# Optimization experiments

Hardware: AMD Instinct MI355X
Metric: run time of the kernel (lower is better)

Reference implementation:

```python
import math
import jax, jax.numpy as jnp
import numpy as np

B, S, HID = 2, 2048, 1024
NH, HD = 16, 64            # num heads, head dim (HID = NH*HD)
NB, MAXD = 32, 128         # relative attention buckets / max distance
Q_SCALING = 1.0


def setup_inputs() -> dict:
    key = jax.random.key(0)
    ks = jax.random.split(key, 6)
    return {
        "hidden_states": jax.random.normal(ks[0], (B, S, HID), dtype=jnp.float32),
        "w_qkv": jax.random.normal(ks[1], (HID, 3 * HID), dtype=jnp.float32) * 0.02,
        "b_qkv": jax.random.normal(ks[2], (3 * HID,), dtype=jnp.float32) * 0.02,
        "w_dense": jax.random.normal(ks[3], (HID, HID), dtype=jnp.float32) * 0.02,
        "b_dense": jax.random.normal(ks[4], (HID,), dtype=jnp.float32) * 0.02,
        "rel_attn_table": jax.random.normal(ks[5], (NH, NB), dtype=jnp.float32) * 0.02,
    }


def _relative_position_bucket(q_len, k_len, num_buckets, max_distance):
    # Bidirectional T5-style buckets, matching compute_relative_bias.
    ctx = jnp.arange(q_len, dtype=jnp.int32)[:, None]
    mem = jnp.arange(k_len, dtype=jnp.int32)[None, :]
    rel = mem - ctx                                     # [Q, K]
    nb = num_buckets // 2
    buckets = jnp.where(rel > 0, nb, 0)
    rel = jnp.abs(rel)
    max_exact = nb // 2
    is_small = rel < max_exact
    # log path (clamp to >=1 to avoid log(0); masked by is_small anyway)
    tmp = jnp.log(jnp.maximum(rel, 1).astype(jnp.float32) / max_exact)
    large = tmp / math.log(max_distance / max_exact) * (nb - max_exact)
    large = max_exact + large.astype(jnp.int32)
    large = jnp.minimum(large, nb - 1)
    return buckets + jnp.where(is_small, rel, large)    # [Q, K]


def reference(hidden_states, w_qkv, b_qkv, w_dense, b_dense, rel_attn_table):
    b, s, _ = hidden_states.shape
    qkv = hidden_states @ w_qkv + b_qkv                 # [B, S, 3*HID]
    q, k, v = jnp.split(qkv, 3, axis=-1)
    q = q.reshape(b, s, NH, HD)
    k = k.reshape(b, s, NH, HD)
    v = v.reshape(b, s, NH, HD)

    norm = Q_SCALING * math.sqrt(HD)
    scores = jnp.einsum("bqhd,bkhd->bhqk", q, k) / norm  # [B, H, S, S]

    buckets = _relative_position_bucket(s, s, NB, MAXD)  # [Q, K] int32
    bias = rel_attn_table[:, buckets]                    # [H, Q, K]
    scores = scores + bias[None]

    probs = jax.nn.softmax(scores, axis=-1)
    ctx = jnp.einsum("bhqk,bkhd->bqhd", probs, v).reshape(b, s, HID)
    return ctx @ w_dense + b_dense
```

## Files before the change

### kernel.cpp

```cpp
#include <hip/hip_runtime.h>
#include <hip/hip_bf16.h>
#include <math.h>

#define S_ 2048

typedef __attribute__((ext_vector_type(8))) short bf16x8;
typedef __attribute__((ext_vector_type(4))) float f32x4;
typedef __attribute__((ext_vector_type(8))) unsigned short u16x8;
typedef __attribute__((ext_vector_type(4))) unsigned short u16x4;

__device__ inline unsigned short f2bf(float f) {
  union { float f; unsigned u; } x; x.f = f;
  unsigned r = x.u + 0x7fff + ((x.u >> 16) & 1);
  return (unsigned short)(r >> 16);
}

__device__ __forceinline__ float exp2_raw(float x) {
  float r;
  asm("v_exp_f32 %0, %1" : "=v"(r) : "v"(x));
  return r;
}

__device__ __forceinline__ void gll16(const unsigned short* g, unsigned short* l) {
  __builtin_amdgcn_global_load_lds(
      (const __attribute__((address_space(1))) unsigned int*)g,
      (__attribute__((address_space(3))) unsigned int*)l, 16, 0, 0);
}

__device__ __forceinline__ void transpose_tile(
    const float* __restrict__ in, unsigned short* __restrict__ out,
    int K, int N, int bx, int by, int tid, unsigned short (*tile)[72]) {
  const int k0 = by * 64, n0 = bx * 64;
  const int rr = tid >> 4, cc = (tid & 15) * 4;
#pragma unroll
  for (int p = 0; p < 4; ++p) {
    int k = rr + p * 16;
    float4 v = *(const float4*)&in[(size_t)(k0 + k) * N + n0 + cc];
    tile[k][cc + 0] = f2bf(v.x);
    tile[k][cc + 1] = f2bf(v.y);
    tile[k][cc + 2] = f2bf(v.z);
    tile[k][cc + 3] = f2bf(v.w);
  }
  __syncthreads();
#pragma unroll
  for (int p = 0; p < 4; ++p) {
    int n = rr + p * 16;
    u16x4 o;
    o[0] = tile[cc + 0][n];
    o[1] = tile[cc + 1][n];
    o[2] = tile[cc + 2][n];
    o[3] = tile[cc + 3][n];
    *(u16x4*)&out[(size_t)(n0 + n) * K + k0 + cc] = o;
  }
}

__global__ __launch_bounds__(256) void prologue_kernel(
    const float* __restrict__ hs, unsigned short* __restrict__ hsb,
    const float* __restrict__ w_qkv, unsigned short* __restrict__ wqT,
    const float* __restrict__ w_dense, unsigned short* __restrict__ wdT,
    const float* __restrict__ table, float* __restrict__ biasTab) {
  __shared__ unsigned short tile[64][72];
  const int blk = blockIdx.x;
  const int tid = threadIdx.x;
  if (blk < 2048) {
    int i = blk * 256 + tid;
    float4 a = ((const float4*)hs)[i * 2];
    float4 b = ((const float4*)hs)[i * 2 + 1];
    u16x8 o;
    o[0] = f2bf(a.x); o[1] = f2bf(a.y); o[2] = f2bf(a.z); o[3] = f2bf(a.w);
    o[4] = f2bf(b.x); o[5] = f2bf(b.y); o[6] = f2bf(b.z); o[7] = f2bf(b.w);
    *(u16x8*)&hsb[(size_t)i * 8] = o;
  } else if (blk < 2816) {
    int t = blk - 2048;
    transpose_tile(w_qkv, wqT, 1024, 3072, t % 48, t / 48, tid, tile);
  } else if (blk < 3072) {
    int t = blk - 2816;
    transpose_tile(w_dense, wdT, 1024, 1024, t % 16, t / 16, tid, tile);
  } else {
    int idx = (blk - 3072) * 256 + tid;
    int h = idx >> 12;
    int r = idx & 4095;
    int rel = r - 2047;
    int bucket = rel > 0 ? 16 : 0;
    int ar = rel < 0 ? -rel : rel;
    if (ar < 8) {
      bucket += ar;
    } else {
      float tmp = logf((float)ar / 8.0f);
      float lf = tmp / 2.7725887222397811f * 8.0f;
      int large = 8 + (int)lf;
      bucket += (large < 15 ? large : 15);
    }
    biasTab[idx] = table[h * 32 + bucket] * 1.44269504088896f;
  }
}

template <bool BF16OUT>
__global__ __launch_bounds__(256) void gemm_mfma_kernel(
    const unsigned short* __restrict__ A, const unsigned short* __restrict__ Bt,
    const float* __restrict__ bias, void* __restrict__ Cout,
    unsigned short* __restrict__ vP, int M, int N, int K) {
  __shared__ __align__(16) unsigned short As[2 * 128 * 32];
  __shared__ __align__(16) unsigned short Bs[2 * 128 * 32];
  const int tid = threadIdx.x;
  const int wave = tid >> 6, lane = tid & 63;
  const int lg = lane >> 4, lr = lane & 15;
  const int nbx = gridDim.x;
  const int flat = blockIdx.y * nbx + blockIdx.x;
  const int cpx = (nbx * gridDim.y) >> 3;
  const int swzid = (flat & 7) * cpx + (flat >> 3);
  const int m0 = (swzid / nbx) * 128, n0 = (swzid % nbx) * 128;
  const int wm = (wave & 1) * 64, wn = (wave >> 1) * 64;

  f32x4 acc[4][4] = {};

  const int r0 = tid >> 2;
  const int sw = ((tid & 3) ^ (r0 & 3)) << 3;
  const unsigned short* aP0 = A + (size_t)(m0 + r0) * K + sw;
  const unsigned short* aP1 = A + (size_t)(m0 + 64 + r0) * K + sw;
  const unsigned short* bP0 = Bt + (size_t)(n0 + r0) * K + sw;
  const unsigned short* bP1 = Bt + (size_t)(n0 + 64 + r0) * K + sw;
  unsigned short* ldsA0 = &As[(tid & ~63) * 8];
  unsigned short* ldsA1 = &As[(256 + (tid & ~63)) * 8];
  unsigned short* ldsB0 = &Bs[(tid & ~63) * 8];
  unsigned short* ldsB1 = &Bs[(256 + (tid & ~63)) * 8];

  const int swz = (lg ^ (lr & 3)) << 3;
  const int NT = K >> 5;

  gll16(aP0, ldsA0);
  gll16(aP1, ldsA1);
  gll16(bP0, ldsB0);
  gll16(bP1, ldsB1);

  for (int ti = 0; ti < NT; ++ti) {
    const int cur = ti & 1;
    __syncthreads();
    if (ti + 1 < NT) {
      const int kt = (ti + 1) << 5;
      const int nb = (cur ^ 1) * 4096;
      gll16(aP0 + kt, ldsA0 + nb);
      gll16(aP1 + kt, ldsA1 + nb);
      gll16(bP0 + kt, ldsB0 + nb);
      gll16(bP1 + kt, ldsB1 + nb);
    }
    const unsigned short* Ab = &As[cur * 4096];
    const unsigned short* Bb = &Bs[cur * 4096];
    bf16x8 af[4], bfr[4];
#pragma unroll
    for (int t = 0; t < 4; ++t) {
      af[t]  = *(const bf16x8*)&Ab[(wm + t * 16 + lr) * 32 + swz];
      bfr[t] = *(const bf16x8*)&Bb[(wn + t * 16 + lr) * 32 + swz];
    }
#pragma unroll
    for (int i = 0; i < 4; ++i)
#pragma unroll
      for (int j = 0; j < 4; ++j)
        acc[i][j] = __builtin_amdgcn_mfma_f32_16x16x32_bf16(
            af[i], bfr[j], acc[i][j], 0, 0, 0);
  }

  float bv[4];
#pragma unroll
  for (int j = 0; j < 4; ++j) bv[j] = bias[n0 + wn + j * 16 + lr];

  if constexpr (BF16OUT) {
    __syncthreads();
    if (n0 < 2048) {
      unsigned short* rp = &As[wave * 1024];
#pragma unroll
      for (int i = 0; i < 4; ++i) {
#pragma unroll
        for (int j = 0; j < 4; ++j) {
          const int cw = ((j + lg) & 3) * 16 + lr;
#pragma unroll
          for (int r = 0; r < 4; ++r)
            rp[(lg * 4 + r) * 64 + cw] = f2bf(acc[i][j][r] + bv[j]);
        }
#pragma unroll
        for (int pass = 0; pass < 2; ++pass) {
          const int row = pass * 8 + (lane >> 3);
          const int cread = ((((lane & 7) >> 1) + (row >> 2)) & 3) * 16 +
                            (lane & 1) * 8;
          u16x8 v = *(const u16x8*)&rp[row * 64 + cread];
          *(u16x8*)&((unsigned short*)Cout)[
              (size_t)(m0 + wm + i * 16 + row) * N + n0 + wn + (lane & 7) * 8] = v;
        }
      }
    } else {
      unsigned short* R = (wave < 2) ? &As[(wave & 1) * 4096]
                                     : &Bs[(wave & 1) * 4096];
#pragma unroll
      for (int i = 0; i < 4; ++i) {
        const int lsv = (i >> 1) * 4 + lg;
        const int ebase = (i & 1) * 4;
#pragma unroll
        for (int j = 0; j < 4; ++j) {
          const int d = j * 16 + lr;
          const int ps = lsv ^ (d & 7);
          u16x4 o;
#pragma unroll
          for (int r = 0; r < 4; ++r) o[r] = f2bf(acc[i][j][r] + bv[j]);
          *(u16x4*)&R[d * 64 + ps * 8 + ebase] = o;
        }
      }
      const int krow0 = m0 + wm;
      const int bbv = krow0 >> 11;
      const int sbase = krow0 & 2047;
      const int h = ((n0 - 2048) >> 6) + (wave >> 1);
#pragma unroll
      for (int it = 0; it < 8; ++it) {
        const int d = it * 8 + (lane >> 3);
        const int c = lane & 7;
        u16x8 v = *(const u16x8*)&R[d * 64 + c * 8];
        *(u16x8*)&vP[((size_t)((bbv * 16 + h) * 64 + d)) * 2048 +
                     sbase + c * 8] = v;
      }
    }
  } else {
#pragma unroll
    for (int i = 0; i < 4; ++i)
#pragma unroll
      for (int j = 0; j < 4; ++j)
#pragma unroll
        for (int r = 0; r < 4; ++r) {
          int row = m0 + wm + i * 16 + lg * 4 + r;
          int col = n0 + wn + j * 16 + lr;
          ((float*)Cout)[(size_t)row * N + col] = acc[i][j][r] + bv[j];
        }
  }
}

template <bool BF16OUT>
__global__ __launch_bounds__(256) void gemm_mfma64_kernel(
    const unsigned short* __restrict__ A, const unsigned short* __restrict__ Bt,
    const float* __restrict__ bias, void* __restrict__ Cout,
    int M, int N, int K) {
  __shared__ __align__(16) unsigned short As[2 * 64 * 32];
  __shared__ __align__(16) unsigned short Bs[2 * 128 * 32];
  const int tid = threadIdx.x;
  const int wave = tid >> 6, lane = tid & 63;
  const int lg = lane >> 4, lr = lane & 15;
  const int nbx = gridDim.x;
  const int flat = blockIdx.y * nbx + blockIdx.x;
  const int cpx = (nbx * gridDim.y) >> 3;
  const int swzid = (flat & 7) * cpx + (flat >> 3);
  const int m0 = (swzid / nbx) * 64, n0 = (swzid % nbx) * 128;
  const int wm = (wave & 1) * 32, wn = (wave >> 1) * 64;

  f32x4 acc[2][4] = {};

  const int r0 = tid >> 2;
  const int sw = ((tid & 3) ^ (r0 & 3)) << 3;
  const unsigned short* aP  = A + (size_t)(m0 + r0) * K + sw;
  const unsigned short* bP0 = Bt + (size_t)(n0 + r0) * K + sw;
  const unsigned short* bP1 = Bt + (size_t)(n0 + 64 + r0) * K + sw;
  unsigned short* ldsA  = &As[(tid & ~63) * 8];
  unsigned short* ldsB0 = &Bs[(tid & ~63) * 8];
  unsigned short* ldsB1 = &Bs[(256 + (tid & ~63)) * 8];

  const int swz = (lg ^ (lr & 3)) << 3;
  const int NT = K >> 5;

  gll16(aP, ldsA);
  gll16(bP0, ldsB0);
  gll16(bP1, ldsB1);

  for (int ti = 0; ti < NT; ++ti) {
    const int cur = ti & 1;
    __syncthreads();
    if (ti + 1 < NT) {
      const int kt = (ti + 1) << 5;
      gll16(aP + kt, ldsA + (cur ^ 1) * 2048);
      gll16(bP0 + kt, ldsB0 + (cur ^ 1) * 4096);
      gll16(bP1 + kt, ldsB1 + (cur ^ 1) * 4096);
    }
    const unsigned short* Ab = &As[cur * 2048];
    const unsigned short* Bb = &Bs[cur * 4096];
    bf16x8 af[2], bfr[4];
#pragma unroll
    for (int t = 0; t < 2; ++t)
      af[t] = *(const bf16x8*)&Ab[(wm + t * 16 + lr) * 32 + swz];
#pragma unroll
    for (int t = 0; t < 4; ++t)
      bfr[t] = *(const bf16x8*)&Bb[(wn + t * 16 + lr) * 32 + swz];
#pragma unroll
    for (int i = 0; i < 2; ++i)
#pragma unroll
      for (int j = 0; j < 4; ++j)
        acc[i][j] = __builtin_amdgcn_mfma_f32_16x16x32_bf16(
            af[i], bfr[j], acc[i][j], 0, 0, 0);
  }

  float bv[4];
#pragma unroll
  for (int j = 0; j < 4; ++j) bv[j] = bias[n0 + wn + j * 16 + lr];
#pragma unroll
  for (int i = 0; i < 2; ++i) {
#pragma unroll
    for (int j = 0; j < 4; ++j) {
#pragma unroll
      for (int r = 0; r < 4; ++r) {
        int row = m0 + wm + i * 16 + lg * 4 + r;
        int col = n0 + wn + j * 16 + lr;
        float val = acc[i][j][r] + bv[j];
        if constexpr (BF16OUT)
          ((unsigned short*)Cout)[(size_t)row * N + col] = f2bf(val);
        else
          ((float*)Cout)[(size_t)row * N + col] = val;
      }
    }
  }
}

__global__ __launch_bounds__(512) void attn_mfma6_kernel(
    const unsigned short* __restrict__ qkvb, const unsigned short* __restrict__ vP,
    const float* __restrict__ biasTab, unsigned short* __restrict__ ctxb) {
  const int wg0 = blockIdx.x;
  const int wg = (wg0 & 7) * 64 + (wg0 >> 3);
  const int qt = wg & 15;
  const int h  = (wg >> 4) & 15;
  const int bb = wg >> 8;

  const int tid = threadIdx.x;
  const int wave = tid >> 6;
  const int lane = tid & 63;
  const int lg = lane >> 4;
  const int lr = lane & 15;

  __shared__ __align__(16) unsigned short Klds[2][4096];
  __shared__ __align__(16) unsigned short Vlds[2][4096];
  __shared__ float biasW[2][192];

  const int q0 = qt * 128;
  const int qw = q0 + wave * 16;
  const float SCL = 0.125f * 1.44269504088896f;
  const float THR = 11.5415603f;

  bf16x8 qf[2];
#pragma unroll
  for (int kh = 0; kh < 2; ++kh)
    qf[kh] = *(const bf16x8*)(qkvb +
        (size_t)(bb * S_ + qw + lr) * 3072 + h * 64 + kh * 32 + lg * 8);

  float mrun = -1e30f;
  float lpart = 0.f;
  f32x4 ov[4] = {};

  const int kk = tid >> 3, kpb = tid & 7;
  const unsigned short* kptr = qkvb + (size_t)(bb * S_ + kk) * 3072 + 1024 +
                               h * 64 + (kpb ^ (kk & 7)) * 8;
  const unsigned short* vptr = vP + ((size_t)((bb * 16 + h) * 64 + (tid >> 3))) * S_ +
                               (tid & 7) * 8;
  const float* btabH = biasTab + h * 4096 + 2047;

  auto nonuni = [&](int tt) {
    int rl = tt * 64 - q0;
    return !((rl - 127 >= 91) || (rl + 63 <= -91));
  };

  gll16(kptr, &Klds[0][(tid & ~63) * 8]);
  gll16(vptr, &Vlds[0][(tid & ~63) * 8]);
  if (nonuni(0) && tid < 192) biasW[0][tid] = btabH[-q0 - 127 + tid];

  for (int t = 0; t < 32; ++t) {
    const int cur = t & 1;
    __syncthreads();

    if (t < 31) {
      const size_t kadv = (size_t)(t + 1) * 64 * 3072;
      gll16(kptr + kadv, &Klds[cur ^ 1][(tid & ~63) * 8]);
      gll16(vptr + (t + 1) * 64, &Vlds[cur ^ 1][(tid & ~63) * 8]);
      if (nonuni(t + 1) && tid < 192)
        biasW[cur ^ 1][tid] = btabH[(t + 1) * 64 - q0 - 127 + tid];
    }

    f32x4 sc[4] = {};
    __builtin_amdgcn_s_setprio(1);
#pragma unroll
    for (int kt = 0; kt < 4; ++kt) {
      const unsigned short* kr = &Klds[cur][(kt * 16 + lr) * 64];
      bf16x8 kf0 = *(const bf16x8*)(kr + ((lg)     ^ (lr & 7)) * 8);
      bf16x8 kf1 = *(const bf16x8*)(kr + ((4 + lg) ^ (lr & 7)) * 8);
      sc[kt] = __builtin_amdgcn_mfma_f32_16x16x32_bf16(kf0, qf[0], sc[kt], 0, 0, 0);
      sc[kt] = __builtin_amdgcn_mfma_f32_16x16x32_bf16(kf1, qf[1], sc[kt], 0, 0, 0);
    }
    __builtin_amdgcn_s_setprio(0);

    bf16x8 vfr[2][4];
#pragma unroll
    for (int kh = 0; kh < 2; ++kh)
#pragma unroll
      for (int db = 0; db < 4; ++db)
        vfr[kh][db] = *(const bf16x8*)&Vlds[cur][
            (db * 16 + lr) * 64 + ((4 * kh + lg) ^ (lr & 7)) * 8];

    float pp[4][4];
    if (nonuni(t)) {
      const int bidx = 127 + lg * 4 - wave * 16 - lr;
#pragma unroll
      for (int kt = 0; kt < 4; ++kt)
#pragma unroll
        for (int r = 0; r < 4; ++r)
          pp[kt][r] = sc[kt][r] * SCL + biasW[cur][bidx + kt * 16 + r];
    } else {
      const float cb = btabH[t * 64 - q0];
#pragma unroll
      for (int kt = 0; kt < 4; ++kt)
#pragma unroll
        for (int r = 0; r < 4; ++r)
          pp[kt][r] = sc[kt][r] * SCL + cb;
    }

    float mx[8];
#pragma unroll
    for (int i = 0; i < 8; ++i)
      mx[i] = fmaxf(pp[i >> 1][(i & 1) * 2], pp[i >> 1][(i & 1) * 2 + 1]);
    float m01 = fmaxf(mx[0], mx[1]), m23 = fmaxf(mx[2], mx[3]);
    float m45 = fmaxf(mx[4], mx[5]), m67 = fmaxf(mx[6], mx[7]);
    float tm = fmaxf(fmaxf(m01, m23), fmaxf(m45, m67));

    if (!__all(tm <= mrun + THR)) {
      tm = fmaxf(tm, __shfl_xor(tm, 16));
      tm = fmaxf(tm, __shfl_xor(tm, 32));
      float mn = fmaxf(mrun, tm);
      float sfv = exp2_raw(mrun - mn);
      mrun = mn;
      lpart *= sfv;
#pragma unroll
      for (int r = 0; r < 4; ++r) {
        float sq = __shfl(sfv, (lane & 48) | (lg * 4 + r));
#pragma unroll
        for (int db = 0; db < 4; ++db) ov[db][r] *= sq;
      }
    }

#pragma unroll
    for (int kt = 0; kt < 4; ++kt)
#pragma unroll
      for (int r = 0; r < 4; ++r)
        pp[kt][r] = exp2_raw(pp[kt][r] - mrun);
    float s8[8];
#pragma unroll
    for (int i = 0; i < 8; ++i)
      s8[i] = pp[i >> 1][(i & 1) * 2] + pp[i >> 1][(i & 1) * 2 + 1];
    float s01 = s8[0] + s8[1], s23 = s8[2] + s8[3];
    float s45 = s8[4] + s8[5], s67 = s8[6] + s8[7];
    lpart += (s01 + s23) + (s45 + s67);

    union { bf16x8 v; unsigned u[4]; } pk[2];
#pragma unroll
    for (int kh = 0; kh < 2; ++kh) {
      asm("v_cvt_pk_bf16_f32 %0, %1, %2"
          : "=v"(pk[kh].u[0]) : "v"(pp[2 * kh][0]), "v"(pp[2 * kh][1]));
      asm("v_cvt_pk_bf16_f32 %0, %1, %2"
          : "=v"(pk[kh].u[1]) : "v"(pp[2 * kh][2]), "v"(pp[2 * kh][3]));
      asm("v_cvt_pk_bf16_f32 %0, %1, %2"
          : "=v"(pk[kh].u[2]) : "v"(pp[2 * kh + 1][0]), "v"(pp[2 * kh + 1][1]));
      asm("v_cvt_pk_bf16_f32 %0, %1, %2"
          : "=v"(pk[kh].u[3]) : "v"(pp[2 * kh + 1][2]), "v"(pp[2 * kh + 1][3]));
    }

    __builtin_amdgcn_s_setprio(1);
#pragma unroll
    for (int kh = 0; kh < 2; ++kh)
#pragma unroll
      for (int db = 0; db < 4; ++db)
        ov[db] = __builtin_amdgcn_mfma_f32_16x16x32_bf16(
            pk[kh].v, vfr[kh][db], ov[db], 0, 0, 0);
    __builtin_amdgcn_s_setprio(0);
  }

  float lsum = lpart;
  lsum += __shfl_xor(lsum, 16);
  lsum += __shfl_xor(lsum, 32);
  float invl = 1.0f / lsum;
#pragma unroll
  for (int r = 0; r < 4; ++r) {
    float iv = __shfl(invl, (lane & 48) | (lg * 4 + r));
    size_t row = (size_t)(bb * S_ + qw + lg * 4 + r);
#pragma unroll
    for (int db = 0; db < 4; ++db)
      ctxb[row * 1024 + h * 64 + db * 16 + lr] = f2bf(ov[db][r] * iv);
  }
}

extern "C" void kernel_launch(void* const* d_in, const int* in_sizes, int n_in,
                              void* d_out, int out_size, void* d_ws, size_t ws_size,
                              hipStream_t stream) {
  const float* hs      = (const float*)d_in[0];
  const float* w_qkv   = (const float*)d_in[1];
  const float* b_qkv   = (const float*)d_in[2];
  const float* w_dense = (const float*)d_in[3];
  const float* b_dense = (const float*)d_in[4];
  const float* rtab    = (const float*)d_in[5];
  float* out = (float*)d_out;

  char* ws = (char*)d_ws;
  unsigned short* qkvb = (unsigned short*)ws;
  unsigned short* ctxb = (unsigned short*)(ws + (((size_t)24) << 20));
  unsigned short* hsb  = (unsigned short*)(ws + (((size_t)32) << 20));
  unsigned short* wqT  = (unsigned short*)(ws + (((size_t)40) << 20));
  unsigned short* wdT  = (unsigned short*)(ws + (((size_t)46) << 20));
  unsigned short* vP   = (unsigned short*)(ws + (((size_t)48) << 20));
  float* biasTab       = (float*)(ws + (((size_t)56) << 20));

  hipLaunchKernelGGL(prologue_kernel, dim3(3328), dim3(256), 0, stream,
                     hs, hsb, w_qkv, wqT, w_dense, wdT, rtab, biasTab);
  hipLaunchKernelGGL((gemm_mfma_kernel<true>), dim3(24, 32), dim3(256), 0, stream,
                     hsb, wqT, b_qkv, (void*)qkvb, vP, 4096, 3072, 1024);
  hipLaunchKernelGGL(attn_mfma6_kernel, dim3(512), dim3(512), 0, stream,
                     qkvb, vP, biasTab, ctxb);
  hipLaunchKernelGGL((gemm_mfma64_kernel<false>), dim3(8, 64), dim3(256), 0, stream,
                     ctxb, wdT, b_dense, (void*)out, 4096, 1024, 1024);
}
```

Baseline: 133.2 us.

## Triple-buffer GEMM LDS tiles with two-deep prefetch and vmcnt waits

Both MFMA GEMM kernels move from double-buffered to triple-buffered LDS staging. Each iteration issues global-to-LDS loads two K-tiles ahead, waits with a partial s_waitcnt vmcnt plus a raw barrier instead of a full __syncthreads, and the bias load is hoisted before the loop. The aim is to hide global load latency behind more MFMA work. In exchange LDS use per block grows by half, which may lower occupancy, and correctness now depends on the hand-written vmcnt counts.

```diff
diff --git a/kernel.cpp b/kernel.cpp
--- a/kernel.cpp
+++ b/kernel.cpp
@@ -100,8 +100,8 @@
     const unsigned short* __restrict__ A, const unsigned short* __restrict__ Bt,
     const float* __restrict__ bias, void* __restrict__ Cout,
     unsigned short* __restrict__ vP, int M, int N, int K) {
-  __shared__ __align__(16) unsigned short As[2 * 128 * 32];
-  __shared__ __align__(16) unsigned short Bs[2 * 128 * 32];
+  __shared__ __align__(16) unsigned short As[3 * 128 * 32];
+  __shared__ __align__(16) unsigned short Bs[3 * 128 * 32];
   const int tid = threadIdx.x;
   const int wave = tid >> 6, lane = tid & 63;
   const int lg = lane >> 4, lr = lane & 15;
@@ -114,38 +114,33 @@
 
   f32x4 acc[4][4] = {};
 
+  float bv[4];
+#pragma unroll
+  for (int j = 0; j < 4; ++j) bv[j] = bias[n0 + wn + j * 16 + lr];
+  asm volatile("" : "+v"(bv[0]), "+v"(bv[1]), "+v"(bv[2]), "+v"(bv[3]));
+
   const int r0 = tid >> 2;
   const int sw = ((tid & 3) ^ (r0 & 3)) << 3;
   const unsigned short* aP0 = A + (size_t)(m0 + r0) * K + sw;
   const unsigned short* aP1 = A + (size_t)(m0 + 64 + r0) * K + sw;
   const unsigned short* bP0 = Bt + (size_t)(n0 + r0) * K + sw;
   const unsigned short* bP1 = Bt + (size_t)(n0 + 64 + r0) * K + sw;
-  unsigned short* ldsA0 = &As[(tid & ~63) * 8];
-  unsigned short* ldsA1 = &As[(256 + (tid & ~63)) * 8];
-  unsigned short* ldsB0 = &Bs[(tid & ~63) * 8];
-  unsigned short* ldsB1 = &Bs[(256 + (tid & ~63)) * 8];
+  const int dstoff = (tid & ~63) * 8;
 
   const int swz = (lg ^ (lr & 3)) << 3;
   const int NT = K >> 5;
 
-  gll16(aP0, ldsA0);
-  gll16(aP1, ldsA1);
-  gll16(bP0, ldsB0);
-  gll16(bP1, ldsB1);
-
-  for (int ti = 0; ti < NT; ++ti) {
-    const int cur = ti & 1;
-    __syncthreads();
-    if (ti + 1 < NT) {
-      const int kt = (ti + 1) << 5;
-      const int nb = (cur ^ 1) * 4096;
-      gll16(aP0 + kt, ldsA0 + nb);
-      gll16(aP1 + kt, ldsA1 + nb);
-      gll16(bP0 + kt, ldsB0 + nb);
-      gll16(bP1 + kt, ldsB1 + nb);
-    }
-    const unsigned short* Ab = &As[cur * 4096];
-    const unsigned short* Bb = &Bs[cur * 4096];
+  auto STAGE = [&](int b, int kt) {
+    unsigned short* Ab = &As[b * 4096];
+    unsigned short* Bb = &Bs[b * 4096];
+    gll16(aP0 + kt, Ab + dstoff);
+    gll16(aP1 + kt, Ab + 2048 + dstoff);
+    gll16(bP0 + kt, Bb + dstoff);
+    gll16(bP1 + kt, Bb + 2048 + dstoff);
+  };
+  auto COMPUTE = [&](int b) {
+    const unsigned short* Ab = &As[b * 4096];
+    const unsigned short* Bb = &Bs[b * 4096];
     bf16x8 af[4], bfr[4];
 #pragma unroll
     for (int t = 0; t < 4; ++t) {
@@ -158,11 +153,25 @@
       for (int j = 0; j < 4; ++j)
         acc[i][j] = __builtin_amdgcn_mfma_f32_16x16x32_bf16(
             af[i], bfr[j], acc[i][j], 0, 0, 0);
-  }
-
-  float bv[4];
-#pragma unroll
-  for (int j = 0; j < 4; ++j) bv[j] = bias[n0 + wn + j * 16 + lr];
+  };
+
+  STAGE(0, 0);
+  STAGE(1, 32);
+
+  int bcur = 0;
+  for (int ti = 0; ti < NT - 1; ++ti) {
+    asm volatile("s_waitcnt vmcnt(4)" ::: "memory");
+    __builtin_amdgcn_s_barrier();
+    if (ti + 2 < NT) {
+      const int bs = bcur >= 1 ? bcur - 1 : 2;
+      STAGE(bs, (ti + 2) << 5);
+    }
+    COMPUTE(bcur);
+    bcur = bcur + 1 < 3 ? bcur + 1 : 0;
+  }
+  asm volatile("s_waitcnt vmcnt(0)" ::: "memory");
+  __builtin_amdgcn_s_barrier();
+  COMPUTE(bcur);
 
   if constexpr (BF16OUT) {
     __syncthreads();
@@ -236,8 +245,8 @@
     const unsigned short* __restrict__ A, const unsigned short* __restrict__ Bt,
     const float* __restrict__ bias, void* __restrict__ Cout,
     int M, int N, int K) {
-  __shared__ __align__(16) unsigned short As[2 * 64 * 32];
-  __shared__ __align__(16) unsigned short Bs[2 * 128 * 32];
+  __shared__ __align__(16) unsigned short As[3 * 64 * 32];
+  __shared__ __align__(16) unsigned short Bs[3 * 128 * 32];
   const int tid = threadIdx.x;
   const int wave = tid >> 6, lane = tid & 63;
   const int lg = lane >> 4, lr = lane & 15;
@@ -250,33 +259,29 @@
 
   f32x4 acc[2][4] = {};
 
+  float bv[4];
+#pragma unroll
+  for (int j = 0; j < 4; ++j) bv[j] = bias[n0 + wn + j * 16 + lr];
+  asm volatile("" : "+v"(bv[0]), "+v"(bv[1]), "+v"(bv[2]), "+v"(bv[3]));
+
   const int r0 = tid >> 2;
   const int sw = ((tid & 3) ^ (r0 & 3)) << 3;
   const unsigned short* aP  = A + (size_t)(m0 + r0) * K + sw;
   const unsigned short* bP0 = Bt + (size_t)(n0 + r0) * K + sw;
   const unsigned short* bP1 = Bt + (size_t)(n0 + 64 + r0) * K + sw;
-  unsigned short* ldsA  = &As[(tid & ~63) * 8];
-  unsigned short* ldsB0 = &Bs[(tid & ~63) * 8];
-  unsigned short* ldsB1 = &Bs[(256 + (tid & ~63)) * 8];
+  const int dstoff = (tid & ~63) * 8;
 
   const int swz = (lg ^ (lr & 3)) << 3;
   const int NT = K >> 5;
 
-  gll16(aP, ldsA);
-  gll16(bP0, ldsB0);
-  gll16(bP1, ldsB1);
-
-  for (int ti = 0; ti < NT; ++ti) {
-    const int cur = ti & 1;
-    __syncthreads();
-    if (ti + 1 < NT) {
-      const int kt = (ti + 1) << 5;
-      gll16(aP + kt, ldsA + (cur ^ 1) * 2048);
-      gll16(bP0 + kt, ldsB0 + (cur ^ 1) * 4096);
-      gll16(bP1 + kt, ldsB1 + (cur ^ 1) * 4096);
-    }
-    const unsigned short* Ab = &As[cur * 2048];
-    const unsigned short* Bb = &Bs[cur * 4096];
+  auto STAGE = [&](int b, int kt) {
+    gll16(aP + kt, &As[b * 2048] + dstoff);
+    gll16(bP0 + kt, &Bs[b * 4096] + dstoff);
+    gll16(bP1 + kt, &Bs[b * 4096 + 2048] + dstoff);
+  };
+  auto COMPUTE = [&](int b) {
+    const unsigned short* Ab = &As[b * 2048];
+    const unsigned short* Bb = &Bs[b * 4096];
     bf16x8 af[2], bfr[4];
 #pragma unroll
     for (int t = 0; t < 2; ++t)
@@ -290,11 +295,26 @@
       for (int j = 0; j < 4; ++j)
         acc[i][j] = __builtin_amdgcn_mfma_f32_16x16x32_bf16(
             af[i], bfr[j], acc[i][j], 0, 0, 0);
-  }
-
-  float bv[4];
-#pragma unroll
-  for (int j = 0; j < 4; ++j) bv[j] = bias[n0 + wn + j * 16 + lr];
+  };
+
+  STAGE(0, 0);
+  STAGE(1, 32);
+
+  int bcur = 0;
+  for (int ti = 0; ti < NT - 1; ++ti) {
+    asm volatile("s_waitcnt vmcnt(3)" ::: "memory");
+    __builtin_amdgcn_s_barrier();
+    if (ti + 2 < NT) {
+      const int bs = bcur >= 1 ? bcur - 1 : 2;
+      STAGE(bs, (ti + 2) << 5);
+    }
+    COMPUTE(bcur);
+    bcur = bcur + 1 < 3 ? bcur + 1 : 0;
+  }
+  asm volatile("s_waitcnt vmcnt(0)" ::: "memory");
+  __builtin_amdgcn_s_barrier();
+  COMPUTE(bcur);
+
 #pragma unroll
   for (int i = 0; i < 2; ++i) {
 #pragma unroll
```

Result: no change. 132.7 us (-0.3%).
